# Kernel optimization log

Measured on AMD Instinct MI355X. Metric: run time of the kernel, lower is better.

The kernel has to match this reference:

```python
import jax, jax.numpy as jnp
import numpy as np

IN_CH = 256
OUT_CH = 64
HEADS = 8


def setup_inputs() -> dict:
    key = jax.random.key(0)
    ks = jax.random.split(key, 7)
    N = 4096
    proj = OUT_CH * HEADS
    s_in = 1.0 / np.sqrt(IN_CH)
    return {
        "query_input": jax.random.normal(ks[0], (N, IN_CH), dtype=jnp.float32),
        "Wq": jax.random.uniform(ks[1], (proj, IN_CH), jnp.float32, -s_in, s_in),
        "bq": jax.random.uniform(ks[2], (proj,), jnp.float32, -s_in, s_in),
        "Wk": jax.random.uniform(ks[3], (proj, IN_CH), jnp.float32, -s_in, s_in),
        "bk": jax.random.uniform(ks[4], (proj,), jnp.float32, -s_in, s_in),
        "Wv": jax.random.uniform(ks[5], (proj, IN_CH), jnp.float32, -s_in, s_in),
        "bv": jax.random.uniform(ks[6], (proj,), jnp.float32, -s_in, s_in),
    }


def reference(query_input, Wq, bq, Wk, bk, Wv, bv):
    N = query_input.shape[0]
    # projections -> [N, H, M]
    q = (query_input @ Wq.T + bq).reshape(N, HEADS, OUT_CH)
    k = (query_input @ Wk.T + bk).reshape(N, HEADS, OUT_CH)
    v = (query_input @ Wv.T + bv).reshape(N, HEADS, OUT_CH)
    # sigmoid attention scores [N, L, H]
    attention_num = jax.nn.sigmoid(jnp.einsum('nhm,lhm->nlh', q, k))
    # sum-normalization over L (keys)
    normalizer = attention_num.sum(axis=1, keepdims=True)  # [N, 1, H]
    attention = attention_num / normalizer
    # weighted V reduction [N, H, D], then mean over heads -> [N, D]
    out = jnp.einsum('nlh,lhd->nhd', attention, v).mean(axis=1)
    return out
```

## Files before the change

kernel.cpp:

```cpp
#include <hip/hip_runtime.h>
#include <hip/hip_bf16.h>
#include <math.h>

#define N_TOK 4096
#define IN_CH 256
#define OUT_CH 64
#define HEADS 8
#define PROJ (OUT_CH * HEADS)
#define NLOG2E -1.44269504088896340736f

typedef float f32x4 __attribute__((ext_vector_type(4)));
typedef __bf16 bf16x8 __attribute__((ext_vector_type(8)));
typedef unsigned short ushort_t;

__device__ inline ushort_t bf16rne(float x) {
    unsigned u = __float_as_uint(x);
    unsigned r = (u + 0x7FFFu + ((u >> 16) & 1u)) >> 16;
    return (ushort_t)r;
}

__global__ __launch_bounds__(256) void cast_pack_kernel(
    const float* __restrict__ X,
    const float* __restrict__ Wq, const float* __restrict__ Wk,
    const float* __restrict__ Wv,
    ushort_t* __restrict__ Xa, ushort_t* __restrict__ Wp)
{
    const int i = blockIdx.x * 256 + threadIdx.x;
    const float* src;
    ushort_t* dst;
    float scale = 1.0f;
    if (i < 131072) {
        const int t = i & 15, quad = (i >> 4) & 3, k8 = (i >> 6) & 7, g = i >> 9;
        src = X + (size_t)(g * 16 + t) * IN_CH + k8 * 32 + quad * 8;
        dst = Xa + (size_t)i * 8;
    } else {
        const int j = i - 131072;
        const int z = j >> 14;
        const int r = j & 16383;
        const int cl = r & 15, quad = (r >> 4) & 3, k8 = (r >> 6) & 7, gc = r >> 9;
        const float* W = (z == 0) ? Wq : (z == 1) ? Wk : Wv;
        src = W + (size_t)(gc * 16 + cl) * IN_CH + k8 * 32 + quad * 8;
        dst = Wp + (size_t)z * 131072 * 8 + (size_t)r * 8;
        if (z == 0) scale = NLOG2E;
    }
    float4 a = *(const float4*)src;
    float4 b = *(const float4*)(src + 4);
    ushort_t pk[8];
    pk[0] = bf16rne(a.x * scale); pk[1] = bf16rne(a.y * scale);
    pk[2] = bf16rne(a.z * scale); pk[3] = bf16rne(a.w * scale);
    pk[4] = bf16rne(b.x * scale); pk[5] = bf16rne(b.y * scale);
    pk[6] = bf16rne(b.z * scale); pk[7] = bf16rne(b.w * scale);
    *(uint4*)dst = *(uint4*)pk;
}

__global__ __launch_bounds__(256) void proj_mfma_kernel(
    const ushort_t* __restrict__ Xa, const ushort_t* __restrict__ Wp,
    const float* __restrict__ bq, const float* __restrict__ bk,
    const float* __restrict__ bv,
    ushort_t* __restrict__ Qb, ushort_t* __restrict__ Kb,
    ushort_t* __restrict__ Vt)
{
    const int z = blockIdx.z;
    const float* bias = (z == 0) ? bq : (z == 1) ? bk : bv;
    const float bscale = (z == 0) ? NLOG2E : 1.0f;
    const int c0 = blockIdx.x * 64;
    const int n0 = blockIdx.y * 64;

    const int tid = threadIdx.x;
    const int w = tid >> 6;
    const int lane = tid & 63;
    const int l15 = lane & 15;
    const int quad = lane >> 4;

    __shared__ ushort_t Es[64 * 68];

    const ushort_t* xa = Xa + (size_t)(blockIdx.y * 4 + w) * 4096 + quad * 128 + l15 * 8;
    const ushort_t* wp0 = Wp + (size_t)z * 131072 * 8 +
                          (size_t)(blockIdx.x * 4) * 4096 + quad * 128 + l15 * 8;

    f32x4 acc[4] = {{0.f, 0.f, 0.f, 0.f}, {0.f, 0.f, 0.f, 0.f},
                    {0.f, 0.f, 0.f, 0.f}, {0.f, 0.f, 0.f, 0.f}};

#pragma unroll 2
    for (int k8 = 0; k8 < 8; ++k8) {
        bf16x8 a = *(const bf16x8*)(xa + k8 * 512);
#pragma unroll
        for (int f = 0; f < 4; ++f) {
            bf16x8 b = *(const bf16x8*)(wp0 + f * 4096 + k8 * 512);
            acc[f] = __builtin_amdgcn_mfma_f32_16x16x32_bf16(a, b, acc[f], 0, 0, 0);
        }
    }

    if (z < 2) {
#pragma unroll
        for (int f = 0; f < 4; ++f) {
            const float bb = bias[c0 + f * 16 + l15] * bscale;
#pragma unroll
            for (int r = 0; r < 4; ++r)
                Es[(w * 16 + quad * 4 + r) * 68 + f * 16 + l15] = bf16rne(acc[f][r] + bb);
        }
    } else {
#pragma unroll
        for (int f = 0; f < 4; ++f) {
            const float bb = bias[c0 + f * 16 + l15];
#pragma unroll
            for (int r = 0; r < 4; ++r)
                Es[(f * 16 + l15) * 68 + w * 16 + quad * 4 + r] = bf16rne(acc[f][r] + bb);
        }
    }
    __syncthreads();

    const int erow = tid >> 2;
    const int ecol = (tid & 3) * 16;
    uint4 pk0 = *(uint4*)&Es[erow * 68 + ecol];
    uint4 pk1 = *(uint4*)&Es[erow * 68 + ecol + 8];
    if (z < 2) {
        ushort_t* out = z ? Kb : Qb;
        ushort_t* p = &out[(size_t)(n0 + erow) * PROJ + c0 + ecol];
        *(uint4*)p = pk0;
        *(uint4*)(p + 8) = pk1;
    } else {
        ushort_t* p = &Vt[(size_t)(c0 + erow) * N_TOK + n0 + ecol];
        *(uint4*)p = pk0;
        *(uint4*)(p + 8) = pk1;
    }
}

template<int ZS>
__global__ __launch_bounds__(256, 4) void attn_kernel(
    const ushort_t* __restrict__ Qb, const ushort_t* __restrict__ Kb,
    const ushort_t* __restrict__ Vt,
    float* __restrict__ NUM, float* __restrict__ DEN)
{
    constexpr int KEYS = N_TOK / ZS;
    constexpr int TILES = KEYS / 64;

    const int h = blockIdx.y;
    const int z = blockIdx.z;
    const int n0 = blockIdx.x * 64;
    const int tid = threadIdx.x;
    const int w = tid >> 6;
    const int lane = tid & 63;
    const int l15 = lane & 15;
    const int quad = lane >> 4;

    __shared__ ushort_t Ks[64 * 64];
    __shared__ ushort_t Vs[64 * 64];
    __shared__ ushort_t Ps[4][16 * 72];

    bf16x8 qb[2];
    {
        const ushort_t* base = Qb + (size_t)(n0 + w * 16 + l15) * PROJ + h * 64 + quad * 8;
        qb[0] = *(const bf16x8*)(base);
        qb[1] = *(const bf16x8*)(base + 32);
    }

    bf16x8 onesv;
#pragma unroll
    for (int j = 0; j < 8; ++j) onesv[j] = (__bf16)1.0f;

    f32x4 o[4] = {{0.f, 0.f, 0.f, 0.f}, {0.f, 0.f, 0.f, 0.f},
                  {0.f, 0.f, 0.f, 0.f}, {0.f, 0.f, 0.f, 0.f}};
    f32x4 dacc = {0.f, 0.f, 0.f, 0.f};

    const int srow = tid >> 2;
    const int sc2 = (tid & 3) * 2;
    const int sp0 = (sc2 ^ (srow & 7)) * 8;
    const int sp1 = ((sc2 + 1) ^ (srow & 7)) * 8;
    const int xm = l15 & 7;
    const int rofA = (quad ^ xm) * 8;
    const int rofB = ((4 + quad) ^ xm) * 8;

    const ushort_t* kgp = Kb + (size_t)h * 64 + sc2 * 8 +
                          (size_t)(z * KEYS + srow) * PROJ;
    const ushort_t* vgp = Vt + (size_t)h * 64 * N_TOK + (size_t)srow * N_TOK +
                          sc2 * 8 + z * KEYS;

    uint4 kr0 = ((const uint4*)kgp)[0], kr1 = ((const uint4*)kgp)[1];
    uint4 vr0 = ((const uint4*)vgp)[0], vr1 = ((const uint4*)vgp)[1];

    for (int lt = 0; lt < TILES; ++lt) {
        __syncthreads();
        *(uint4*)&Ks[srow * 64 + sp0] = kr0;
        *(uint4*)&Ks[srow * 64 + sp1] = kr1;
        *(uint4*)&Vs[srow * 64 + sp0] = vr0;
        *(uint4*)&Vs[srow * 64 + sp1] = vr1;
        __syncthreads();

        if (lt < TILES - 1) {
            kgp += 64 * PROJ;
            vgp += 64;
            kr0 = ((const uint4*)kgp)[0]; kr1 = ((const uint4*)kgp)[1];
            vr0 = ((const uint4*)vgp)[0]; vr1 = ((const uint4*)vgp)[1];
        }

        f32x4 s[4] = {{0.f, 0.f, 0.f, 0.f}, {0.f, 0.f, 0.f, 0.f},
                      {0.f, 0.f, 0.f, 0.f}, {0.f, 0.f, 0.f, 0.f}};
        __builtin_amdgcn_s_setprio(1);
#pragma unroll
        for (int f = 0; f < 4; ++f) {
            bf16x8 ka = *(const bf16x8*)&Ks[(f * 16 + l15) * 64 + rofA];
            s[f] = __builtin_amdgcn_mfma_f32_16x16x32_bf16(ka, qb[0], s[f], 0, 0, 0);
        }
#pragma unroll
        for (int f = 0; f < 4; ++f) {
            bf16x8 ka = *(const bf16x8*)&Ks[(f * 16 + l15) * 64 + rofB];
            s[f] = __builtin_amdgcn_mfma_f32_16x16x32_bf16(ka, qb[1], s[f], 0, 0, 0);
        }
        __builtin_amdgcn_s_setprio(0);

        ushort_t* pw = &Ps[w][l15 * 72];
#pragma unroll
        for (int f = 0; f < 4; ++f) {
            float p0 = __builtin_amdgcn_rcpf(1.0f + __builtin_amdgcn_exp2f(s[f][0]));
            float p1 = __builtin_amdgcn_rcpf(1.0f + __builtin_amdgcn_exp2f(s[f][1]));
            float p2 = __builtin_amdgcn_rcpf(1.0f + __builtin_amdgcn_exp2f(s[f][2]));
            float p3 = __builtin_amdgcn_rcpf(1.0f + __builtin_amdgcn_exp2f(s[f][3]));
            unsigned u0 = __float_as_uint(p0) + 0x8000u;
            unsigned u1 = __float_as_uint(p1) + 0x8000u;
            unsigned u2 = __float_as_uint(p2) + 0x8000u;
            unsigned u3 = __float_as_uint(p3) + 0x8000u;
            uint2 pk;
            pk.x = __builtin_amdgcn_perm(u1, u0, 0x07060302u);
            pk.y = __builtin_amdgcn_perm(u3, u2, 0x07060302u);
            *(uint2*)&pw[f * 16 + quad * 4] = pk;
        }

        __builtin_amdgcn_s_setprio(1);
#pragma unroll
        for (int c = 0; c < 2; ++c) {
            bf16x8 pa = *(const bf16x8*)&Ps[w][l15 * 72 + c * 32 + quad * 8];
            const int rof = c ? rofB : rofA;
#pragma unroll
            for (int f = 0; f < 4; ++f) {
                bf16x8 vb = *(const bf16x8*)&Vs[(f * 16 + l15) * 64 + rof];
                o[f] = __builtin_amdgcn_mfma_f32_16x16x32_bf16(pa, vb, o[f], 0, 0, 0);
            }
            dacc = __builtin_amdgcn_mfma_f32_16x16x32_bf16(pa, onesv, dacc, 0, 0, 0);
        }
        __builtin_amdgcn_s_setprio(0);
    }

#pragma unroll
    for (int f = 0; f < 4; ++f) {
#pragma unroll
        for (int r = 0; r < 4; ++r) {
            const int q = n0 + w * 16 + quad * 4 + r;
            NUM[((size_t)z * N_TOK + q) * PROJ + h * 64 + f * 16 + l15] = o[f][r];
        }
    }
    if (l15 == 0) {
#pragma unroll
        for (int r = 0; r < 4; ++r)
            DEN[((size_t)z * N_TOK + n0 + w * 16 + quad * 4 + r) * HEADS + h] = dacc[r];
    }
}

template<int ZS>
__global__ __launch_bounds__(256) void reduce_kernel(
    const float* __restrict__ NUM, const float* __restrict__ DEN,
    float* __restrict__ out)
{
    const int g = blockIdx.x * 256 + threadIdx.x;
    const int n = g >> 6;
    const int d = g & 63;
    float acc = 0.0f;
#pragma unroll
    for (int hh = 0; hh < HEADS; ++hh) {
        float num = 0.0f, dd = 0.0f;
#pragma unroll
        for (int zz = 0; zz < ZS; ++zz) {
            num += NUM[((size_t)zz * N_TOK + n) * PROJ + hh * 64 + d];
            dd  += DEN[((size_t)zz * N_TOK + n) * HEADS + hh];
        }
        acc += num / dd;
    }
    out[g] = acc * 0.125f;
}

extern "C" void kernel_launch(void* const* d_in, const int* in_sizes, int n_in,
                              void* d_out, int out_size, void* d_ws, size_t ws_size,
                              hipStream_t stream) {
    (void)in_sizes; (void)n_in; (void)out_size;
    const float* X  = (const float*)d_in[0];
    const float* Wq = (const float*)d_in[1];
    const float* bq = (const float*)d_in[2];
    const float* Wk = (const float*)d_in[3];
    const float* bk = (const float*)d_in[4];
    const float* Wv = (const float*)d_in[5];
    const float* bv = (const float*)d_in[6];
    float* out = (float*)d_out;

    const size_t NEED4 =
        (size_t)4 * N_TOK * PROJ * 4 + (size_t)4 * N_TOK * HEADS * 4 +
        (size_t)3 * N_TOK * PROJ * 2 + (size_t)N_TOK * IN_CH * 2 +
        (size_t)3 * PROJ * IN_CH * 2;
    const int ZS = (ws_size >= NEED4) ? 4 : 2;

    float* NUM = (float*)d_ws;
    float* DEN = NUM + (size_t)ZS * N_TOK * PROJ;
    ushort_t* Qb = (ushort_t*)(DEN + (size_t)ZS * N_TOK * HEADS);
    ushort_t* Kb = Qb + (size_t)N_TOK * PROJ;
    ushort_t* Vt = Kb + (size_t)N_TOK * PROJ;
    ushort_t* Xa = Vt + (size_t)N_TOK * PROJ;
    ushort_t* Wp = Xa + (size_t)N_TOK * IN_CH;

    cast_pack_kernel<<<dim3(704), 256, 0, stream>>>(X, Wq, Wk, Wv, Xa, Wp);
    proj_mfma_kernel<<<dim3(PROJ / 64, N_TOK / 64, 3), 256, 0, stream>>>(
        Xa, Wp, bq, bk, bv, Qb, Kb, Vt);
    if (ZS == 4) {
        attn_kernel<4><<<dim3(N_TOK / 64, HEADS, 4), 256, 0, stream>>>(
            Qb, Kb, Vt, NUM, DEN);
        reduce_kernel<4><<<dim3(N_TOK * OUT_CH / 256), 256, 0, stream>>>(
            NUM, DEN, out);
    } else {
        attn_kernel<2><<<dim3(N_TOK / 64, HEADS, 2), 256, 0, stream>>>(
            Qb, Kb, Vt, NUM, DEN);
        reduce_kernel<2><<<dim3(N_TOK * OUT_CH / 256), 256, 0, stream>>>(
            NUM, DEN, out);
    }
}
```

Baseline: 142.8 us.

## Switch attention to 32x32x16 MFMA with 128-query tiles and scalar denominator

Reworks the attention kernel to use 32x32x16 bf16 MFMA instructions, with each wave owning 32 queries so a block covers 128 queries. The grid x dimension is halved accordingly. Each K/V tile loaded into shared memory now serves twice as many queries, cutting LDS fill and global K/V traffic per query. The denominator is now summed in registers from the fp32 sigmoid values plus one cross-half shuffle, replacing the extra MFMA against a ones vector. In exchange, accumulators grow to two 16-wide vectors per wave, which raises register pressure, and the grid has fewer blocks.

```diff
diff --git a/kernel.cpp b/kernel.cpp
--- a/kernel.cpp
+++ b/kernel.cpp
@@ -10,6 +10,7 @@
 #define NLOG2E -1.44269504088896340736f
 
 typedef float f32x4 __attribute__((ext_vector_type(4)));
+typedef float f32x16 __attribute__((ext_vector_type(16)));
 typedef __bf16 bf16x8 __attribute__((ext_vector_type(8)));
 typedef unsigned short ushort_t;
 
@@ -137,39 +138,35 @@
 
     const int h = blockIdx.y;
     const int z = blockIdx.z;
-    const int n0 = blockIdx.x * 64;
+    const int n0 = blockIdx.x * 128;
     const int tid = threadIdx.x;
     const int w = tid >> 6;
     const int lane = tid & 63;
-    const int l15 = lane & 15;
-    const int quad = lane >> 4;
+    const int l31 = lane & 31;
+    const int hf = lane >> 5;
 
     __shared__ ushort_t Ks[64 * 64];
     __shared__ ushort_t Vs[64 * 64];
-    __shared__ ushort_t Ps[4][16 * 72];
-
-    bf16x8 qb[2];
+    __shared__ ushort_t Ps[4][32 * 72];
+
+    bf16x8 qb[4];
     {
-        const ushort_t* base = Qb + (size_t)(n0 + w * 16 + l15) * PROJ + h * 64 + quad * 8;
+        const ushort_t* base = Qb + (size_t)(n0 + w * 32 + l31) * PROJ + h * 64 + hf * 8;
         qb[0] = *(const bf16x8*)(base);
-        qb[1] = *(const bf16x8*)(base + 32);
-    }
-
-    bf16x8 onesv;
-#pragma unroll
-    for (int j = 0; j < 8; ++j) onesv[j] = (__bf16)1.0f;
-
-    f32x4 o[4] = {{0.f, 0.f, 0.f, 0.f}, {0.f, 0.f, 0.f, 0.f},
-                  {0.f, 0.f, 0.f, 0.f}, {0.f, 0.f, 0.f, 0.f}};
-    f32x4 dacc = {0.f, 0.f, 0.f, 0.f};
+        qb[1] = *(const bf16x8*)(base + 16);
+        qb[2] = *(const bf16x8*)(base + 32);
+        qb[3] = *(const bf16x8*)(base + 48);
+    }
+
+    f32x16 o0 = {};
+    f32x16 o1 = {};
+    float den = 0.0f;
 
     const int srow = tid >> 2;
     const int sc2 = (tid & 3) * 2;
     const int sp0 = (sc2 ^ (srow & 7)) * 8;
     const int sp1 = ((sc2 + 1) ^ (srow & 7)) * 8;
-    const int xm = l15 & 7;
-    const int rofA = (quad ^ xm) * 8;
-    const int rofB = ((4 + quad) ^ xm) * 8;
+    const int xm = l31 & 7;
 
     const ushort_t* kgp = Kb + (size_t)h * 64 + sc2 * 8 +
                           (size_t)(z * KEYS + srow) * PROJ;
@@ -178,6 +175,8 @@
 
     uint4 kr0 = ((const uint4*)kgp)[0], kr1 = ((const uint4*)kgp)[1];
     uint4 vr0 = ((const uint4*)vgp)[0], vr1 = ((const uint4*)vgp)[1];
+
+    ushort_t* pw = &Ps[w][l31 * 72];
 
     for (int lt = 0; lt < TILES; ++lt) {
         __syncthreads();
@@ -194,28 +193,26 @@
             vr0 = ((const uint4*)vgp)[0]; vr1 = ((const uint4*)vgp)[1];
         }
 
-        f32x4 s[4] = {{0.f, 0.f, 0.f, 0.f}, {0.f, 0.f, 0.f, 0.f},
-                      {0.f, 0.f, 0.f, 0.f}, {0.f, 0.f, 0.f, 0.f}};
+        f32x16 s0 = {};
+        f32x16 s1 = {};
         __builtin_amdgcn_s_setprio(1);
 #pragma unroll
-        for (int f = 0; f < 4; ++f) {
-            bf16x8 ka = *(const bf16x8*)&Ks[(f * 16 + l15) * 64 + rofA];
-            s[f] = __builtin_amdgcn_mfma_f32_16x16x32_bf16(ka, qb[0], s[f], 0, 0, 0);
-        }
-#pragma unroll
-        for (int f = 0; f < 4; ++f) {
-            bf16x8 ka = *(const bf16x8*)&Ks[(f * 16 + l15) * 64 + rofB];
-            s[f] = __builtin_amdgcn_mfma_f32_16x16x32_bf16(ka, qb[1], s[f], 0, 0, 0);
+        for (int ks = 0; ks < 4; ++ks) {
+            const int pos = ((ks * 2 + hf) ^ xm) * 8;
+            bf16x8 ka0 = *(const bf16x8*)&Ks[l31 * 64 + pos];
+            s0 = __builtin_amdgcn_mfma_f32_32x32x16_bf16(ka0, qb[ks], s0, 0, 0, 0);
+            bf16x8 ka1 = *(const bf16x8*)&Ks[(32 + l31) * 64 + pos];
+            s1 = __builtin_amdgcn_mfma_f32_32x32x16_bf16(ka1, qb[ks], s1, 0, 0, 0);
         }
         __builtin_amdgcn_s_setprio(0);
 
-        ushort_t* pw = &Ps[w][l15 * 72];
-#pragma unroll
-        for (int f = 0; f < 4; ++f) {
-            float p0 = __builtin_amdgcn_rcpf(1.0f + __builtin_amdgcn_exp2f(s[f][0]));
-            float p1 = __builtin_amdgcn_rcpf(1.0f + __builtin_amdgcn_exp2f(s[f][1]));
-            float p2 = __builtin_amdgcn_rcpf(1.0f + __builtin_amdgcn_exp2f(s[f][2]));
-            float p3 = __builtin_amdgcn_rcpf(1.0f + __builtin_amdgcn_exp2f(s[f][3]));
+#pragma unroll
+        for (int rq = 0; rq < 4; ++rq) {
+            float p0 = __builtin_amdgcn_rcpf(1.0f + __builtin_amdgcn_exp2f(s0[rq * 4 + 0]));
+            float p1 = __builtin_amdgcn_rcpf(1.0f + __builtin_amdgcn_exp2f(s0[rq * 4 + 1]));
+            float p2 = __builtin_amdgcn_rcpf(1.0f + __builtin_amdgcn_exp2f(s0[rq * 4 + 2]));
+            float p3 = __builtin_amdgcn_rcpf(1.0f + __builtin_amdgcn_exp2f(s0[rq * 4 + 3]));
+            den += (p0 + p1) + (p2 + p3);
             unsigned u0 = __float_as_uint(p0) + 0x8000u;
             unsigned u1 = __float_as_uint(p1) + 0x8000u;
             unsigned u2 = __float_as_uint(p2) + 0x8000u;
@@ -223,36 +220,51 @@
             uint2 pk;
             pk.x = __builtin_amdgcn_perm(u1, u0, 0x07060302u);
             pk.y = __builtin_amdgcn_perm(u3, u2, 0x07060302u);
-            *(uint2*)&pw[f * 16 + quad * 4] = pk;
+            *(uint2*)&pw[rq * 8 + hf * 4] = pk;
+        }
+#pragma unroll
+        for (int rq = 0; rq < 4; ++rq) {
+            float p0 = __builtin_amdgcn_rcpf(1.0f + __builtin_amdgcn_exp2f(s1[rq * 4 + 0]));
+            float p1 = __builtin_amdgcn_rcpf(1.0f + __builtin_amdgcn_exp2f(s1[rq * 4 + 1]));
+            float p2 = __builtin_amdgcn_rcpf(1.0f + __builtin_amdgcn_exp2f(s1[rq * 4 + 2]));
+            float p3 = __builtin_amdgcn_rcpf(1.0f + __builtin_amdgcn_exp2f(s1[rq * 4 + 3]));
+            den += (p0 + p1) + (p2 + p3);
+            unsigned u0 = __float_as_uint(p0) + 0x8000u;
+            unsigned u1 = __float_as_uint(p1) + 0x8000u;
+            unsigned u2 = __float_as_uint(p2) + 0x8000u;
+            unsigned u3 = __float_as_uint(p3) + 0x8000u;
+            uint2 pk;
+            pk.x = __builtin_amdgcn_perm(u1, u0, 0x07060302u);
+            pk.y = __builtin_amdgcn_perm(u3, u2, 0x07060302u);
+            *(uint2*)&pw[32 + rq * 8 + hf * 4] = pk;
         }
 
         __builtin_amdgcn_s_setprio(1);
 #pragma unroll
-        for (int c = 0; c < 2; ++c) {
-            bf16x8 pa = *(const bf16x8*)&Ps[w][l15 * 72 + c * 32 + quad * 8];
-            const int rof = c ? rofB : rofA;
-#pragma unroll
-            for (int f = 0; f < 4; ++f) {
-                bf16x8 vb = *(const bf16x8*)&Vs[(f * 16 + l15) * 64 + rof];
-                o[f] = __builtin_amdgcn_mfma_f32_16x16x32_bf16(pa, vb, o[f], 0, 0, 0);
-            }
-            dacc = __builtin_amdgcn_mfma_f32_16x16x32_bf16(pa, onesv, dacc, 0, 0, 0);
+        for (int ks = 0; ks < 4; ++ks) {
+            bf16x8 pa = *(const bf16x8*)&Ps[w][l31 * 72 + ks * 16 + hf * 8];
+            const int pos = ((ks * 2 + hf) ^ xm) * 8;
+            bf16x8 vb0 = *(const bf16x8*)&Vs[l31 * 64 + pos];
+            o0 = __builtin_amdgcn_mfma_f32_32x32x16_bf16(pa, vb0, o0, 0, 0, 0);
+            bf16x8 vb1 = *(const bf16x8*)&Vs[(32 + l31) * 64 + pos];
+            o1 = __builtin_amdgcn_mfma_f32_32x32x16_bf16(pa, vb1, o1, 0, 0, 0);
         }
         __builtin_amdgcn_s_setprio(0);
     }
 
 #pragma unroll
-    for (int f = 0; f < 4; ++f) {
-#pragma unroll
-        for (int r = 0; r < 4; ++r) {
-            const int q = n0 + w * 16 + quad * 4 + r;
-            NUM[((size_t)z * N_TOK + q) * PROJ + h * 64 + f * 16 + l15] = o[f][r];
-        }
-    }
-    if (l15 == 0) {
-#pragma unroll
-        for (int r = 0; r < 4; ++r)
-            DEN[((size_t)z * N_TOK + n0 + w * 16 + quad * 4 + r) * HEADS + h] = dacc[r];
+    for (int rq = 0; rq < 4; ++rq) {
+#pragma unroll
+        for (int j = 0; j < 4; ++j) {
+            const int q = n0 + w * 32 + rq * 8 + hf * 4 + j;
+            float* p = &NUM[((size_t)z * N_TOK + q) * PROJ + h * 64 + l31];
+            p[0]  = o0[rq * 4 + j];
+            p[32] = o1[rq * 4 + j];
+        }
+    }
+    den += __shfl_xor(den, 32);
+    if (lane < 32) {
+        DEN[((size_t)z * N_TOK + n0 + w * 32 + lane) * HEADS + h] = den;
     }
 }
 
@@ -309,12 +321,12 @@
     proj_mfma_kernel<<<dim3(PROJ / 64, N_TOK / 64, 3), 256, 0, stream>>>(
         Xa, Wp, bq, bk, bv, Qb, Kb, Vt);
     if (ZS == 4) {
-        attn_kernel<4><<<dim3(N_TOK / 64, HEADS, 4), 256, 0, stream>>>(
+        attn_kernel<4><<<dim3(N_TOK / 128, HEADS, 4), 256, 0, stream>>>(
             Qb, Kb, Vt, NUM, DEN);
         reduce_kernel<4><<<dim3(N_TOK * OUT_CH / 256), 256, 0, stream>>>(
             NUM, DEN, out);
     } else {
-        attn_kernel<2><<<dim3(N_TOK / 64, HEADS, 2), 256, 0, stream>>>(
+        attn_kernel<2><<<dim3(N_TOK / 128, HEADS, 2), 256, 0, stream>>>(
             Qb, Kb, Vt, NUM, DEN);
         reduce_kernel<2><<<dim3(N_TOK * OUT_CH / 256), 256, 0, stream>>>(
             NUM, DEN, out);
```

Result: no change. 145.0 us (+1.5%).
